# Kernel optimization log

Hardware: AMD Instinct MI355X
Metric: run time of the kernel (lower is better)

The kernel has to match this reference:

```python
import jax, jax.numpy as jnp
import numpy as np

D = 1024
NH = 16
DH = D // NH
B = 2
N = 2048
EPS = 1e-5


def setup_inputs() -> dict:
    key = jax.random.key(0)
    ks = jax.random.split(key, 12)
    s = 0.02
    return {
        "x": jax.random.normal(ks[0], (B, N, D), jnp.float32),
        "Wq": jax.random.normal(ks[1], (D, D), jnp.float32) * s,
        "Wk": jax.random.normal(ks[2], (D, D), jnp.float32) * s,
        "Wv": jax.random.normal(ks[3], (D, D), jnp.float32) * s,
        "Wo": jax.random.normal(ks[4], (D, D), jnp.float32) * s,
        "bo": jnp.zeros((D,), jnp.float32),
        "ln1_scale": jnp.ones((D,), jnp.float32),
        "ln1_shift": jnp.zeros((D,), jnp.float32),
        "ln2_scale": jnp.ones((D,), jnp.float32),
        "ln2_shift": jnp.zeros((D,), jnp.float32),
        "W1": jax.random.normal(ks[5], (4 * D, D), jnp.float32) * s,
        "b1": jnp.zeros((4 * D,), jnp.float32),
        "W2": jax.random.normal(ks[6], (D, 4 * D), jnp.float32) * s,
        "b2": jnp.zeros((D,), jnp.float32),
    }


def _layernorm(x, scale, shift):
    mean = jnp.mean(x, axis=-1, keepdims=True)
    var = jnp.mean(jnp.square(x - mean), axis=-1, keepdims=True)  # unbiased=False
    return scale * ((x - mean) / jnp.sqrt(var + EPS)) + shift


def _gelu(x):
    c = jnp.sqrt(jnp.asarray(2.0 / jnp.pi, x.dtype))
    return 0.5 * x * (1.0 + jnp.tanh(c * (x + 0.044715 * x * x * x)))


def reference(x, Wq, Wk, Wv, Wo, bo, ln1_scale, ln1_shift, ln2_scale, ln2_shift, W1, b1, W2, b2):
    Bx, Nx, d = x.shape
    # pre-MHA LN
    h = _layernorm(x, ln1_scale, ln1_shift)
    # projections (torch Linear: y = h @ W.T), no bias for Wq/Wk/Wv
    q = (h @ Wq.T).reshape(Bx, Nx, NH, DH).transpose(0, 2, 1, 3)  # [B,nh,N,dh]
    k = (h @ Wk.T).reshape(Bx, Nx, NH, DH).transpose(0, 2, 1, 3)
    v = (h @ Wv.T).reshape(Bx, Nx, NH, DH).transpose(0, 2, 1, 3)
    s = jnp.einsum("bhnd,bhmd->bhnm", q, k)  # [B,nh,N,N]
    causal = jnp.tril(jnp.ones((Nx, Nx), bool))
    s = jnp.where(causal, s, -jnp.inf)
    p = jax.nn.softmax(s / jnp.sqrt(jnp.asarray(DH, s.dtype)), axis=-1)
    pv = jnp.einsum("bhnm,bhmd->bhnd", p, v)
    pv = pv.transpose(0, 2, 1, 3).reshape(Bx, Nx, d)
    attn = pv @ Wo.T + bo
    x = x + attn  # residual (dropout is identity, dpo=0)
    # pre-FFN LN + FFN
    h = _layernorm(x, ln2_scale, ln2_shift)
    h = _gelu(h @ W1.T + b1)
    h = h @ W2.T + b2
    return x + h
```

## Files before the change

kernel.cpp:

```cpp
#include <hip/hip_runtime.h>
#include <hip/hip_bf16.h>
#include <math.h>

#define Dmod   1024
#define NHmod  16
#define DHmod  64
#define Bmod   2
#define Nmod   2048
#define Mrows  (Bmod * Nmod)
#define FF     (4 * Dmod)
#define EPSLN  1e-5f

typedef __attribute__((ext_vector_type(8))) short bf16x8;
typedef __attribute__((ext_vector_type(4))) float f32x4;
typedef unsigned short ushort_t;
typedef unsigned int uint_t;

#define MFMA16x16x32(a, b, c) __builtin_amdgcn_mfma_f32_16x16x32_bf16((a), (b), (c), 0, 0, 0)

#define AS1 __attribute__((address_space(1)))
#define AS3 __attribute__((address_space(3)))

__device__ __forceinline__ void gload_lds16(const ushort_t* g, ushort_t* l) {
    __builtin_amdgcn_global_load_lds((const AS1 uint_t*)(const void*)g,
                                     (AS3 uint_t*)(void*)l, 16, 0, 0);
}

__device__ __forceinline__ ushort_t f2bf(float f) {
    union { float f; uint_t u; } v; v.f = f;
    uint_t r = v.u + 0x7FFFu + ((v.u >> 16) & 1u);
    return (ushort_t)(r >> 16);
}

__device__ __forceinline__ float bf2f(uint_t u) {
    union { float f; uint_t u; } v; v.u = u << 16;
    return v.f;
}

__global__ __launch_bounds__(256) void cvt_kernel(const float* __restrict__ Wq, const float* __restrict__ Wk,
                                                  const float* __restrict__ Wv, const float* __restrict__ Wo,
                                                  const float* __restrict__ W1, const float* __restrict__ W2,
                                                  ushort_t* __restrict__ qkv, ushort_t* __restrict__ wo,
                                                  ushort_t* __restrict__ w1, ushort_t* __restrict__ w2) {
    int u = blockIdx.x * 256 + threadIdx.x;
    const float* src; ushort_t* dst; int i;
    float scale = 1.0f;
    if (u < 393216) {
        if (u < 131072)      { src = Wq; dst = qkv;           i = u; scale = 0.125f; }
        else if (u < 262144) { src = Wk; dst = qkv + 1048576; i = u - 131072; }
        else                 { src = Wv; dst = qkv + 2097152; i = u - 262144; }
    } else if (u < 524288)   { src = Wo; dst = wo; i = u - 393216; }
    else if (u < 1048576)    { src = W1; dst = w1; i = u - 524288; }
    else                     { src = W2; dst = w2; i = u - 1048576; }
    float4 a = ((const float4*)src)[2 * i];
    float4 b = ((const float4*)src)[2 * i + 1];
    uint4 o;
    o.x = (uint_t)f2bf(a.x * scale) | ((uint_t)f2bf(a.y * scale) << 16);
    o.y = (uint_t)f2bf(a.z * scale) | ((uint_t)f2bf(a.w * scale) << 16);
    o.z = (uint_t)f2bf(b.x * scale) | ((uint_t)f2bf(b.y * scale) << 16);
    o.w = (uint_t)f2bf(b.z * scale) | ((uint_t)f2bf(b.w * scale) << 16);
    ((uint4*)dst)[i] = o;
}

__global__ __launch_bounds__(256) void ln_bf_kernel(const float* __restrict__ x,
                                                    const float* __restrict__ scale,
                                                    const float* __restrict__ shift,
                                                    ushort_t* __restrict__ out) {
    int row = blockIdx.x;
    const float4* xr = (const float4*)(x + (size_t)row * Dmod);
    float4 v = xr[threadIdx.x];
    float s  = v.x + v.y + v.z + v.w;
    float s2 = v.x*v.x + v.y*v.y + v.z*v.z + v.w*v.w;

    __shared__ float rs[8], rs2[8];
    #pragma unroll
    for (int o = 32; o; o >>= 1) { s += __shfl_down(s, o); s2 += __shfl_down(s2, o); }
    int wave = threadIdx.x >> 6, lane = threadIdx.x & 63;
    if (lane == 0) { rs[wave] = s; rs2[wave] = s2; }
    __syncthreads();
    if (threadIdx.x == 0) {
        rs[0]  = rs[0] + rs[1] + rs[2] + rs[3];
        rs2[0] = rs2[0] + rs2[1] + rs2[2] + rs2[3];
    }
    __syncthreads();
    float mean = rs[0] * (1.0f / Dmod);
    float var  = rs2[0] * (1.0f / Dmod) - mean * mean;
    float rstd = rsqrtf(var + EPSLN);

    float4 sc = ((const float4*)scale)[threadIdx.x];
    float4 sh = ((const float4*)shift)[threadIdx.x];
    uint2 o;
    o.x = (uint_t)f2bf(sc.x * (v.x - mean) * rstd + sh.x) |
          ((uint_t)f2bf(sc.y * (v.y - mean) * rstd + sh.y) << 16);
    o.y = (uint_t)f2bf(sc.z * (v.z - mean) * rstd + sh.z) |
          ((uint_t)f2bf(sc.w * (v.w - mean) * rstd + sh.w) << 16);
    ((uint2*)(out + (size_t)row * Dmod))[threadIdx.x] = o;
}

__device__ __forceinline__ float gelu_f(float x) {
    const float c = 0.7978845608028654f;
    float u = c * (x + 0.044715f * x * x * x);
    return x / (1.0f + __expf(-2.0f * u));
}

#define DSR(D, A, OFF) asm volatile("ds_read_b128 %0, %1 offset:" OFF : "=v"(D) : "v"(A))
#define SB0 __builtin_amdgcn_sched_barrier(0)
#define BARR __builtin_amdgcn_s_barrier()
#define LGKM(N) asm volatile("s_waitcnt lgkmcnt(" #N ")" ::)

#define GRP_QM0(J, B) \
  acc[0][J]=MFMA16x16x32(a0,B,acc[0][J]); acc[1][J]=MFMA16x16x32(a1,B,acc[1][J]); \
  acc[2][J]=MFMA16x16x32(a2,B,acc[2][J]); acc[3][J]=MFMA16x16x32(a3,B,acc[3][J]);
#define GRP_QM1(I, A) \
  acc[I][0]=MFMA16x16x32(A,b0,acc[I][0]); acc[I][1]=MFMA16x16x32(A,b1,acc[I][1]); \
  acc[I][2]=MFMA16x16x32(A,b2,acc[I][2]); acc[I][3]=MFMA16x16x32(A,b3,acc[I][3]);

template <int MODE>
__global__ __launch_bounds__(512, 2) void gemm256(const ushort_t* __restrict__ A,
                                                  const ushort_t* __restrict__ W,
                                                  const float* __restrict__ bias,
                                                  void* __restrict__ Cv,
                                                  int M, int Nout, int K, int KS,
                                                  int GN, int GM) {
    __shared__ ushort_t Ab[32768];
    __shared__ ushort_t Bb[32768];
    int tid = threadIdx.x;
    int w  = tid >> 6, l = tid & 63;
    int li = l & 15,  g = l >> 4;
    int wm = w >> 2,  wn = w & 3;

    int xcd = blockIdx.x & 7;
    int c   = blockIdx.x >> 3;
    int RN = GN >> 2, RM = GM >> 1;
    int rsz = RN * RM;
    int bz = c / rsz;
    int r  = c - bz * rsz;
    int bm = (xcd >> 2) * RM + r / RN;
    int bn = (xcd & 3) * RN + r % RN;

    int lc   = (l & 7) ^ (l >> 3);
    int sgr  = w * 32 + 2 * (l >> 3) + (lc >> 2);
    int colo = (lc & 3) * 8;
    const ushort_t* sA0 = A + (size_t)(bm * 256 + sgr) * K + bz * KS + colo;
    const ushort_t* sA1 = sA0 + (size_t)16 * K;
    const ushort_t* sB0 = W + (size_t)(bn * 256 + sgr) * K + bz * KS + colo;
    const ushort_t* sB1 = sB0 + (size_t)16 * K;

    uint_t chunkpos = (uint_t)(((((li & 1) << 2) + g) ^ (li >> 1)) << 4);
    uint_t aBase = (uint_t)(uintptr_t)(&Ab[0]) + (uint_t)(wm * 8192 + (li >> 1) * 128) + chunkpos;
    uint_t bBase = (uint_t)(uintptr_t)(&Bb[0]) + (uint_t)(wn * 4096 + (li >> 1) * 128) + chunkpos;

    f32x4 acc[8][4];
    #pragma unroll
    for (int i = 0; i < 8; i++)
        #pragma unroll
        for (int j = 0; j < 4; j++) acc[i][j] = (f32x4){0.f, 0.f, 0.f, 0.f};

    const int NT = KS >> 6;

    {
        ushort_t* dA = &Ab[0] + w * 1024;
        ushort_t* dB = &Bb[0] + w * 1024;
        gload_lds16(sA0,      dA);        gload_lds16(sA1,      dA + 512);
        gload_lds16(sB0,      dB);        gload_lds16(sB1,      dB + 512);
        gload_lds16(sA0 + 32, dA + 8192); gload_lds16(sA1 + 32, dA + 8192 + 512);
        gload_lds16(sB0 + 32, dB + 8192); gload_lds16(sB1 + 32, dB + 8192 + 512);
    }
    asm volatile("s_waitcnt vmcnt(4)" ::);
    SB0; BARR;

    for (int t = 0; t < NT; ++t) {
        int d = t & 1;
        bool pf = (t + 1 < NT);
        int kn = (t + 1) * 64;
        uint_t aAddr = aBase + (uint_t)(d * 32768);
        uint_t bAddr = bBase + (uint_t)(d * 32768);
        ushort_t* dA = &Ab[0] + (d ^ 1) * 16384 + w * 1024;
        ushort_t* dB = &Bb[0] + (d ^ 1) * 16384 + w * 1024;
        bf16x8 a0, a1, a2, a3, b0, b1, b2, b3;

        DSR(a0, aAddr, "0");    DSR(a1, aAddr, "1024");
        DSR(a2, aAddr, "2048"); DSR(a3, aAddr, "3072");
        DSR(b0, bAddr, "0");    DSR(b1, bAddr, "1024");
        DSR(b2, bAddr, "2048"); DSR(b3, bAddr, "3072");
        if (pf) { gload_lds16(sA0 + kn, dA); gload_lds16(sA1 + kn, dA + 512); }
        SB0; BARR;
        LGKM(3); SB0;
        __builtin_amdgcn_s_setprio(1);
        GRP_QM0(0, b0)
        LGKM(2); SB0;
        GRP_QM0(1, b1)
        LGKM(1); SB0;
        GRP_QM0(2, b2)
        LGKM(0); SB0;
        GRP_QM0(3, b3)
        __builtin_amdgcn_s_setprio(0);
        SB0; BARR;

        DSR(a0, aAddr, "4096"); DSR(a1, aAddr, "5120");
        DSR(a2, aAddr, "6144"); DSR(a3, aAddr, "7168");
        if (pf) { gload_lds16(sB0 + kn, dB); gload_lds16(sB1 + kn, dB + 512); }
        SB0; BARR;
        LGKM(3); SB0;
        __builtin_amdgcn_s_setprio(1);
        GRP_QM1(4, a0)
        LGKM(2); SB0;
        GRP_QM1(5, a1)
        LGKM(1); SB0;
        GRP_QM1(6, a2)
        LGKM(0); SB0;
        GRP_QM1(7, a3)
        __builtin_amdgcn_s_setprio(0);
        if (pf) { asm volatile("s_waitcnt vmcnt(4)" ::); }
        else    { asm volatile("s_waitcnt vmcnt(0)" ::); }
        SB0; BARR;

        DSR(a0, aAddr, "16384"); DSR(a1, aAddr, "17408");
        DSR(a2, aAddr, "18432"); DSR(a3, aAddr, "19456");
        DSR(b0, bAddr, "16384"); DSR(b1, bAddr, "17408");
        DSR(b2, bAddr, "18432"); DSR(b3, bAddr, "19456");
        if (pf) { gload_lds16(sA0 + kn + 32, dA + 8192); gload_lds16(sA1 + kn + 32, dA + 8192 + 512); }
        SB0; BARR;
        LGKM(3); SB0;
        __builtin_amdgcn_s_setprio(1);
        GRP_QM0(0, b0)
        LGKM(2); SB0;
        GRP_QM0(1, b1)
        LGKM(1); SB0;
        GRP_QM0(2, b2)
        LGKM(0); SB0;
        GRP_QM0(3, b3)
        __builtin_amdgcn_s_setprio(0);
        SB0; BARR;

        DSR(a0, aAddr, "20480"); DSR(a1, aAddr, "21504");
        DSR(a2, aAddr, "22528"); DSR(a3, aAddr, "23552");
        if (pf) { gload_lds16(sB0 + kn + 32, dB + 8192); gload_lds16(sB1 + kn + 32, dB + 8192 + 512); }
        SB0; BARR;
        LGKM(3); SB0;
        __builtin_amdgcn_s_setprio(1);
        GRP_QM1(4, a0)
        LGKM(2); SB0;
        GRP_QM1(5, a1)
        LGKM(1); SB0;
        GRP_QM1(6, a2)
        LGKM(0); SB0;
        GRP_QM1(7, a3)
        __builtin_amdgcn_s_setprio(0);
        asm volatile("s_waitcnt vmcnt(4)" ::);
        SB0; BARR;
    }

    #pragma unroll
    for (int fm = 0; fm < 8; fm++) {
        #pragma unroll
        for (int fn = 0; fn < 4; fn++) {
            int nn = bn * 256 + wn * 64 + fn * 16 + li;
            int mB = bm * 256 + wm * 128 + (fm >> 2) * 64 + (fm & 3) * 16 + g * 4;
            if (MODE == 0) {
                int which = nn >> 10, col = nn & 1023;
                int h = col >> 6, dd = col & 63;
                int b = mB >> 11, n0 = mB & (Nmod - 1);
                ushort_t* C = (ushort_t*)Cv;
                if (which == 2) {
                    uint2 pk;
                    pk.x = (uint_t)f2bf(acc[fm][fn][0]) | ((uint_t)f2bf(acc[fm][fn][1]) << 16);
                    pk.y = (uint_t)f2bf(acc[fm][fn][2]) | ((uint_t)f2bf(acc[fm][fn][3]) << 16);
                    *(uint2*)(C + 8388608u + (((size_t)(b * NHmod + h)) * DHmod + dd) * Nmod + n0) = pk;
                } else {
                    #pragma unroll
                    for (int r2 = 0; r2 < 4; r2++) {
                        size_t idx = (size_t)which * 4194304u +
                                     (((size_t)(b * NHmod + h)) * Nmod + n0 + r2) * DHmod + dd;
                        C[idx] = f2bf(acc[fm][fn][r2]);
                    }
                }
            } else if (MODE == 2) {
                ushort_t* C = (ushort_t*)Cv;
                #pragma unroll
                for (int r2 = 0; r2 < 4; r2++)
                    C[(size_t)(mB + r2) * Nout + nn] = f2bf(gelu_f(acc[fm][fn][r2] + bias[nn]));
            } else {
                ushort_t* P = (ushort_t*)Cv + (size_t)bz * M * Nout;
                #pragma unroll
                for (int r2 = 0; r2 < 4; r2++)
                    P[(size_t)(mB + r2) * Nout + nn] = f2bf(acc[fm][fn][r2]);
            }
        }
    }
}

__global__ __launch_bounds__(256) void red_ln4_kernel(const ushort_t* __restrict__ p,
                                                      const float* __restrict__ x,
                                                      const float* __restrict__ bo,
                                                      const float* __restrict__ scale,
                                                      const float* __restrict__ shift,
                                                      float* __restrict__ x1,
                                                      ushort_t* __restrict__ h2) {
    int row = blockIdx.x;
    int t   = threadIdx.x;
    const size_t MD = (size_t)Mrows * Dmod;
    size_t i = (size_t)row * 256 + t;
    float4 xr = ((const float4*)(x + (size_t)row * Dmod))[t];
    float4 bb = ((const float4*)bo)[t];
    float4 v;
    v.x = xr.x + bb.x; v.y = xr.y + bb.y; v.z = xr.z + bb.z; v.w = xr.w + bb.w;
    #pragma unroll
    for (int z = 0; z < 4; z++) {
        uint2 pk = ((const uint2*)(p + (size_t)z * MD))[i];
        v.x += bf2f(pk.x & 0xffffu);
        v.y += bf2f(pk.x >> 16);
        v.z += bf2f(pk.y & 0xffffu);
        v.w += bf2f(pk.y >> 16);
    }
    ((float4*)(x1 + (size_t)row * Dmod))[t] = v;

    float s  = v.x + v.y + v.z + v.w;
    float s2 = v.x*v.x + v.y*v.y + v.z*v.z + v.w*v.w;
    __shared__ float rs[8], rs2[8];
    #pragma unroll
    for (int o = 32; o; o >>= 1) { s += __shfl_down(s, o); s2 += __shfl_down(s2, o); }
    int wave = t >> 6, lane = t & 63;
    if (lane == 0) { rs[wave] = s; rs2[wave] = s2; }
    __syncthreads();
    if (t == 0) {
        rs[0]  = rs[0] + rs[1] + rs[2] + rs[3];
        rs2[0] = rs2[0] + rs2[1] + rs2[2] + rs2[3];
    }
    __syncthreads();
    float mean = rs[0] * (1.0f / Dmod);
    float var  = rs2[0] * (1.0f / Dmod) - mean * mean;
    float rstd = rsqrtf(var + EPSLN);

    float4 sc = ((const float4*)scale)[t];
    float4 sh = ((const float4*)shift)[t];
    uint2 o;
    o.x = (uint_t)f2bf(sc.x * (v.x - mean) * rstd + sh.x) |
          ((uint_t)f2bf(sc.y * (v.y - mean) * rstd + sh.y) << 16);
    o.y = (uint_t)f2bf(sc.z * (v.z - mean) * rstd + sh.z) |
          ((uint_t)f2bf(sc.w * (v.w - mean) * rstd + sh.w) << 16);
    ((uint2*)(h2 + (size_t)row * Dmod))[t] = o;
}

__global__ __launch_bounds__(256) void red_out4_kernel(const ushort_t* __restrict__ p,
                                                       const float* __restrict__ x1,
                                                       const float* __restrict__ b2,
                                                       float* __restrict__ out) {
    const size_t MD4 = (size_t)Mrows * Dmod / 4;
    size_t i = (size_t)blockIdx.x * 256 + threadIdx.x;
    if (i >= MD4) return;
    float4 xr = ((const float4*)x1)[i];
    float4 bb = ((const float4*)b2)[i & 255];
    float4 v;
    v.x = xr.x + bb.x; v.y = xr.y + bb.y; v.z = xr.z + bb.z; v.w = xr.w + bb.w;
    #pragma unroll
    for (int z = 0; z < 4; z++) {
        uint2 pk = ((const uint2*)(p + (size_t)z * Mrows * Dmod))[i];
        v.x += bf2f(pk.x & 0xffffu);
        v.y += bf2f(pk.x >> 16);
        v.z += bf2f(pk.y & 0xffffu);
        v.w += bf2f(pk.y >> 16);
    }
    ((float4*)out)[i] = v;
}

__global__ __launch_bounds__(256) void fattn_kernel(const ushort_t* __restrict__ Q,
                                                    const ushort_t* __restrict__ K,
                                                    const ushort_t* __restrict__ VT,
                                                    ushort_t* __restrict__ O) {
    int bid = blockIdx.x;
    int xcd = bid & 7;
    int j   = bid >> 3;
    int bh  = xcd * 4 + (j & 3);
    int qt  = 31 - (j >> 2);
    int b   = bh >> 4, hh = bh & 15;
    int w    = threadIdx.x >> 6;
    int lane = threadIdx.x & 63;
    int li   = lane & 15;
    int g    = lane >> 4;

    __shared__ ushort_t Klds[2][4096];
    __shared__ ushort_t Vlds[2][4096];
    __shared__ ushort_t Plds[4][16][72];

    int q0 = qt * 64 + w * 16;
    int q  = q0 + li;

    const ushort_t* Qb = Q  + (size_t)bh * Nmod * DHmod;
    const ushort_t* Kb = K  + (size_t)bh * Nmod * DHmod;
    const ushort_t* Vb = VT + (size_t)bh * DHmod * Nmod;

    bf16x8 qf[2];
    #pragma unroll
    for (int c = 0; c < 2; c++)
        qf[c] = *(const bf16x8*)(Qb + (size_t)q * DHmod + c * 32 + g * 8);

    f32x4 po[4];
    #pragma unroll
    for (int mt = 0; mt < 4; mt++) po[mt] = (f32x4){0.f, 0.f, 0.f, 0.f};
    float l = 0.f;

    const int ntiles = qt + 1;

    int r_sub = lane >> 3;
    int cc    = ((lane & 7) ^ (r_sub & 7)) * 8;

    int swz  = (li & 7) * 8;
    int roff = li * 64;
    int c0k  = (g * 8) ^ swz;
    int c1k  = (32 + g * 8) ^ swz;

    auto stage = [&](int buf, int kt) {
        int k0 = kt * 64;
        #pragma unroll
        for (int i2 = 0; i2 < 2; i2++) {
            int i   = w * 2 + i2;
            int row = i * 8 + r_sub;
            gload_lds16(Kb + (size_t)(k0 + row) * DHmod + cc, &Klds[buf][i * 512]);
            gload_lds16(Vb + (size_t)row * Nmod + k0 + cc,    &Vlds[buf][i * 512]);
        }
    };

    stage(0, 0);

    for (int kt = 0; kt < ntiles; ++kt) {
        __syncthreads();
        if (kt + 1 < ntiles) stage((kt + 1) & 1, kt + 1);
        int cur = kt & 1;
        int k0  = kt * 64;

        f32x4 s[4];
        __builtin_amdgcn_s_setprio(1);
        #pragma unroll
        for (int mt = 0; mt < 4; mt++) {
            bf16x8 kf0 = *(const bf16x8*)&Klds[cur][mt * 1024 + roff + c0k];
            bf16x8 kf1 = *(const bf16x8*)&Klds[cur][mt * 1024 + roff + c1k];
            s[mt] = (f32x4){0.f, 0.f, 0.f, 0.f};
            s[mt] = MFMA16x16x32(kf0, qf[0], s[mt]);
            s[mt] = MFMA16x16x32(kf1, qf[1], s[mt]);
        }
        __builtin_amdgcn_s_setprio(0);

        if (kt == qt) {
            #pragma unroll
            for (int mt = 0; mt < 4; mt++)
                #pragma unroll
                for (int r = 0; r < 4; r++)
                    if (k0 + mt * 16 + g * 4 + r > q) s[mt][r] = -INFINITY;
        }
        float ptile = 0.f;
        #pragma unroll
        for (int mt = 0; mt < 4; mt++) {
            float p0 = __expf(s[mt][0]);
            float p1 = __expf(s[mt][1]);
            float p2 = __expf(s[mt][2]);
            float p3 = __expf(s[mt][3]);
            ptile += (p0 + p1) + (p2 + p3);
            uint2 pk;
            pk.x = (uint_t)f2bf(p0) | ((uint_t)f2bf(p1) << 16);
            pk.y = (uint_t)f2bf(p2) | ((uint_t)f2bf(p3) << 16);
            *(uint2*)&Plds[w][li][mt * 16 + g * 4] = pk;
        }
        l += ptile;

        asm volatile("" ::: "memory");

        bf16x8 pf0 = *(const bf16x8*)&Plds[w][li][g * 8];
        bf16x8 pf1 = *(const bf16x8*)&Plds[w][li][32 + g * 8];
        __builtin_amdgcn_s_setprio(1);
        #pragma unroll
        for (int mt = 0; mt < 4; mt++) {
            bf16x8 vf0 = *(const bf16x8*)&Vlds[cur][mt * 1024 + roff + c0k];
            bf16x8 vf1 = *(const bf16x8*)&Vlds[cur][mt * 1024 + roff + c1k];
            po[mt] = MFMA16x16x32(vf0, pf0, po[mt]);
            po[mt] = MFMA16x16x32(vf1, pf1, po[mt]);
        }
        __builtin_amdgcn_s_setprio(0);
        asm volatile("" ::: "memory");
    }

    l += __shfl_xor(l, 16);
    l += __shfl_xor(l, 32);
    float inv = 1.0f / l;
    ushort_t* Orow = O + ((size_t)(b * Nmod + q)) * Dmod + hh * DHmod;
    #pragma unroll
    for (int mt = 0; mt < 4; mt++) {
        uint2 pk;
        pk.x = (uint_t)f2bf(po[mt][0] * inv) | ((uint_t)f2bf(po[mt][1] * inv) << 16);
        pk.y = (uint_t)f2bf(po[mt][2] * inv) | ((uint_t)f2bf(po[mt][3] * inv) << 16);
        *(uint2*)(Orow + mt * 16 + g * 4) = pk;
    }
}

extern "C" void kernel_launch(void* const* d_in, const int* in_sizes, int n_in,
                              void* d_out, int out_size, void* d_ws, size_t ws_size,
                              hipStream_t stream) {
    const float* x    = (const float*)d_in[0];
    const float* Wq   = (const float*)d_in[1];
    const float* Wk   = (const float*)d_in[2];
    const float* Wv   = (const float*)d_in[3];
    const float* Wo   = (const float*)d_in[4];
    const float* bo   = (const float*)d_in[5];
    const float* ln1s = (const float*)d_in[6];
    const float* ln1b = (const float*)d_in[7];
    const float* ln2s = (const float*)d_in[8];
    const float* ln2b = (const float*)d_in[9];
    const float* W1   = (const float*)d_in[10];
    const float* b1   = (const float*)d_in[11];
    const float* W2   = (const float*)d_in[12];
    const float* b2   = (const float*)d_in[13];
    float* out = (float*)d_out;
    char*  wsb = (char*)d_ws;

    ushort_t* h_bf  = (ushort_t*)wsb;
    ushort_t* qb    = (ushort_t*)(wsb + (8u  << 20));
    ushort_t* kb    = qb + 4194304;
    ushort_t* vtb   = qb + 8388608;
    float*    x1    = (float*)(wsb + (32u << 20));
    ushort_t* h2_bf = (ushort_t*)(wsb + (48u << 20));
    ushort_t* g_bf  = (ushort_t*)(wsb + (56u << 20));
    ushort_t* wqkv  = (ushort_t*)(wsb + (88u << 20));
    ushort_t* wo_b  = (ushort_t*)(wsb + (94u << 20));
    ushort_t* w1_b  = (ushort_t*)(wsb + (96u << 20));
    ushort_t* w2_b  = (ushort_t*)(wsb + (104u << 20));
    ushort_t* att   = h_bf;
    ushort_t* pWoB = (ushort_t*)(wsb + (56u << 20));
    ushort_t* pFd  = (ushort_t*)wsb;

    cvt_kernel<<<6144, 256, 0, stream>>>(Wq, Wk, Wv, Wo, W1, W2, wqkv, wo_b, w1_b, w2_b);
    ln_bf_kernel<<<Mrows, 256, 0, stream>>>(x, ln1s, ln1b, h_bf);
    gemm256<0><<<192, 512, 0, stream>>>(h_bf, wqkv, nullptr, qb, Mrows, 3072, Dmod, Dmod, 12, 16);
    fattn_kernel<<<1024, 256, 0, stream>>>(qb, kb, vtb, att);
    gemm256<4><<<256, 512, 0, stream>>>(att, wo_b, nullptr, pWoB, Mrows, Dmod, Dmod, Dmod / 4, 4, 16);
    red_ln4_kernel<<<Mrows, 256, 0, stream>>>(pWoB, x, bo, ln2s, ln2b, x1, h2_bf);
    gemm256<2><<<256, 512, 0, stream>>>(h2_bf, w1_b, b1, g_bf, Mrows, FF, Dmod, Dmod, 16, 16);
    gemm256<4><<<256, 512, 0, stream>>>(g_bf, w2_b, nullptr, pFd, Mrows, Dmod, FF, FF / 4, 4, 16);
    red_out4_kernel<<<(Mrows * Dmod / 4 + 255) / 256, 256, 0, stream>>>(pFd, x1, b2, out);
}
```

Before: 221.0 us.

## Issue whole next K-tile prefetch at once and use one barrier per iteration

The GEMM main loop now issues all eight global-to-LDS loads for the next K tile at the start of each iteration and drops the intra-iteration barriers, keeping only a full vmcnt(0) wait and a single barrier at the end. This removes many workgroup barriers and the staggered partial waits, aiming to cut synchronisation overhead. In exchange, the prefetch can no longer overlap with the next iteration's first reads, since the end-of-iteration wait drains all loads. The staggered schedule that spread load issue across MFMA groups is also lost.

```diff
diff --git a/kernel.cpp b/kernel.cpp
--- a/kernel.cpp
+++ b/kernel.cpp
@@ -158,33 +158,32 @@
 
     const int NT = KS >> 6;
 
-    {
-        ushort_t* dA = &Ab[0] + w * 1024;
-        ushort_t* dB = &Bb[0] + w * 1024;
-        gload_lds16(sA0,      dA);        gload_lds16(sA1,      dA + 512);
-        gload_lds16(sB0,      dB);        gload_lds16(sB1,      dB + 512);
-        gload_lds16(sA0 + 32, dA + 8192); gload_lds16(sA1 + 32, dA + 8192 + 512);
-        gload_lds16(sB0 + 32, dB + 8192); gload_lds16(sB1 + 32, dB + 8192 + 512);
-    }
-    asm volatile("s_waitcnt vmcnt(4)" ::);
+    auto stage_all = [&](int dst, int t) {
+        int kn = t * 64;
+        ushort_t* dA = &Ab[0] + dst * 16384 + w * 1024;
+        ushort_t* dB = &Bb[0] + dst * 16384 + w * 1024;
+        gload_lds16(sA0 + kn,      dA);        gload_lds16(sA1 + kn,      dA + 512);
+        gload_lds16(sB0 + kn,      dB);        gload_lds16(sB1 + kn,      dB + 512);
+        gload_lds16(sA0 + kn + 32, dA + 8192); gload_lds16(sA1 + kn + 32, dA + 8192 + 512);
+        gload_lds16(sB0 + kn + 32, dB + 8192); gload_lds16(sB1 + kn + 32, dB + 8192 + 512);
+    };
+
+    stage_all(0, 0);
+    asm volatile("s_waitcnt vmcnt(0)" ::);
     SB0; BARR;
 
     for (int t = 0; t < NT; ++t) {
         int d = t & 1;
-        bool pf = (t + 1 < NT);
-        int kn = (t + 1) * 64;
         uint_t aAddr = aBase + (uint_t)(d * 32768);
         uint_t bAddr = bBase + (uint_t)(d * 32768);
-        ushort_t* dA = &Ab[0] + (d ^ 1) * 16384 + w * 1024;
-        ushort_t* dB = &Bb[0] + (d ^ 1) * 16384 + w * 1024;
         bf16x8 a0, a1, a2, a3, b0, b1, b2, b3;
 
         DSR(a0, aAddr, "0");    DSR(a1, aAddr, "1024");
         DSR(a2, aAddr, "2048"); DSR(a3, aAddr, "3072");
         DSR(b0, bAddr, "0");    DSR(b1, bAddr, "1024");
         DSR(b2, bAddr, "2048"); DSR(b3, bAddr, "3072");
-        if (pf) { gload_lds16(sA0 + kn, dA); gload_lds16(sA1 + kn, dA + 512); }
-        SB0; BARR;
+        if (t + 1 < NT) stage_all(d ^ 1, t + 1);
+        SB0;
         LGKM(3); SB0;
         __builtin_amdgcn_s_setprio(1);
         GRP_QM0(0, b0)
@@ -195,12 +194,10 @@
         LGKM(0); SB0;
         GRP_QM0(3, b3)
         __builtin_amdgcn_s_setprio(0);
-        SB0; BARR;
 
         DSR(a0, aAddr, "4096"); DSR(a1, aAddr, "5120");
         DSR(a2, aAddr, "6144"); DSR(a3, aAddr, "7168");
-        if (pf) { gload_lds16(sB0 + kn, dB); gload_lds16(sB1 + kn, dB + 512); }
-        SB0; BARR;
+        SB0;
         LGKM(3); SB0;
         __builtin_amdgcn_s_setprio(1);
         GRP_QM1(4, a0)
@@ -211,16 +208,12 @@
         LGKM(0); SB0;
         GRP_QM1(7, a3)
         __builtin_amdgcn_s_setprio(0);
-        if (pf) { asm volatile("s_waitcnt vmcnt(4)" ::); }
-        else    { asm volatile("s_waitcnt vmcnt(0)" ::); }
-        SB0; BARR;
 
         DSR(a0, aAddr, "16384"); DSR(a1, aAddr, "17408");
         DSR(a2, aAddr, "18432"); DSR(a3, aAddr, "19456");
         DSR(b0, bAddr, "16384"); DSR(b1, bAddr, "17408");
         DSR(b2, bAddr, "18432"); DSR(b3, bAddr, "19456");
-        if (pf) { gload_lds16(sA0 + kn + 32, dA + 8192); gload_lds16(sA1 + kn + 32, dA + 8192 + 512); }
-        SB0; BARR;
+        SB0;
         LGKM(3); SB0;
         __builtin_amdgcn_s_setprio(1);
         GRP_QM0(0, b0)
@@ -231,12 +224,10 @@
         LGKM(0); SB0;
         GRP_QM0(3, b3)
         __builtin_amdgcn_s_setprio(0);
-        SB0; BARR;
 
         DSR(a0, aAddr, "20480"); DSR(a1, aAddr, "21504");
         DSR(a2, aAddr, "22528"); DSR(a3, aAddr, "23552");
-        if (pf) { gload_lds16(sB0 + kn + 32, dB + 8192); gload_lds16(sB1 + kn + 32, dB + 8192 + 512); }
-        SB0; BARR;
+        SB0;
         LGKM(3); SB0;
         __builtin_amdgcn_s_setprio(1);
         GRP_QM1(4, a0)
@@ -247,7 +238,8 @@
         LGKM(0); SB0;
         GRP_QM1(7, a3)
         __builtin_amdgcn_s_setprio(0);
-        asm volatile("s_waitcnt vmcnt(4)" ::);
+
+        asm volatile("s_waitcnt vmcnt(0)" ::);
         SB0; BARR;
     }
 
```

Result: no change. 219.4 us (-0.7%).
